# Optimization experiments

Measured on AMD Instinct MI355X. Metric: run time of the kernel, lower is better.

Reference implementation:

```python
import jax, jax.numpy as jnp
import numpy as np

NH = 8       # num_heads
EDIM = 256   # embedding_dim (also per-head dim in this module)
BS, SQL = 4, 1024


def setup_inputs() -> dict:
    key = jax.random.key(0)
    ks = jax.random.split(key, 5)
    scale_in = 1.0 / np.sqrt(EDIM)
    scale_out = 1.0 / np.sqrt(NH * EDIM)
    return {
        "x": jax.random.normal(ks[0], (BS, SQL, EDIM), dtype=jnp.float32),
        "w_attn": jax.random.normal(ks[1], (NH * 3 * EDIM, EDIM), dtype=jnp.float32) * scale_in,
        "b_attn": jax.random.normal(ks[2], (NH * 3 * EDIM,), dtype=jnp.float32) * scale_in,
        "w_out": jax.random.normal(ks[3], (EDIM, NH * EDIM), dtype=jnp.float32) * scale_out,
        "b_out": jax.random.normal(ks[4], (EDIM,), dtype=jnp.float32) * scale_out,
    }


def reference(x, w_attn, b_attn, w_out, b_out):
    bs, sql, edim = x.shape
    nh = NH
    # projections: (bs, sql, nh*3*edim); split into Q, K, V chunks of nh*edim
    proj = x @ w_attn.T + b_attn
    q, k, v = jnp.split(proj, 3, axis=-1)
    # Faithful to torch: raw view (bs, sql, nh*edim) -> (bs, nh, sql, edim),
    # a reinterpretation of memory, NOT a transpose.
    q = q.reshape(bs, nh, sql, edim)
    k = k.reshape(bs, nh, sql, edim)
    v = v.reshape(bs, nh, sql, edim)
    # scaled dot-product scores: (bs, nh, sql, sql)
    scores = jnp.einsum("bhqd,bhkd->bhqk", q, k) / jnp.sqrt(jnp.float32(edim))
    # causal mask: -inf strictly above the diagonal (equivalent to adding triu(-inf, 1))
    causal = jnp.tril(jnp.ones((sql, sql), dtype=bool))
    scores = jnp.where(causal, scores, -jnp.inf)
    attn = jax.nn.softmax(scores, axis=-1)
    out = jnp.einsum("bhqk,bhkd->bhqd", attn, v)
    # Faithful raw view back: (bs, nh, sql, edim) -> (bs, sql, nh*edim)
    out = out.reshape(bs, sql, nh * edim)
    return out @ w_out.T + b_out
```

## Files before the change

### kernel.cpp

```cpp
#include <hip/hip_runtime.h>

#define SQL  1024
#define EDIM 256
#define NHD  8
#define NKV  (NHD * 3 * EDIM)
#define MROWS (4 * SQL)

typedef short bf16x8 __attribute__((ext_vector_type(8)));
typedef float f32x4 __attribute__((ext_vector_type(4)));

__device__ __forceinline__ unsigned short f2bf(float f) {
  unsigned u = __float_as_uint(f);
  u += 0x7fff + ((u >> 16) & 1);
  return (unsigned short)(u >> 16);
}
__device__ __forceinline__ float bf2f(unsigned short s) {
  return __uint_as_float(((unsigned)s) << 16);
}

__device__ __forceinline__ void g2lds16(const void* g, void* l) {
  __builtin_amdgcn_global_load_lds(
      (const __attribute__((address_space(1))) unsigned int*)g,
      (__attribute__((address_space(3))) unsigned int*)l, 16, 0, 0);
}

__device__ __forceinline__ void storev(float* p, float v) { *p = v; }
__device__ __forceinline__ void storev(unsigned short* p, float v) { *p = f2bf(v); }

__global__ __launch_bounds__(256) void cast3_bf16(
    const float* __restrict__ x, unsigned short* __restrict__ xb,
    const float* __restrict__ wa, unsigned short* __restrict__ wb,
    const float* __restrict__ wo, unsigned short* __restrict__ wob) {
  const float* src; unsigned short* dst; int i;
  int blk = blockIdx.x;
  if (blk < 512)       { src = x;  dst = xb;  i = blk * 256 + threadIdx.x; }
  else if (blk < 1280) { src = wa; dst = wb;  i = (blk - 512) * 256 + threadIdx.x; }
  else                 { src = wo; dst = wob; i = (blk - 1280) * 256 + threadIdx.x; }
  float4 a = ((const float4*)src)[2 * i];
  float4 b = ((const float4*)src)[2 * i + 1];
  union { unsigned short s[8]; ulonglong2 v; } u;
  u.s[0] = f2bf(a.x); u.s[1] = f2bf(a.y); u.s[2] = f2bf(a.z); u.s[3] = f2bf(a.w);
  u.s[4] = f2bf(b.x); u.s[5] = f2bf(b.y); u.s[6] = f2bf(b.z); u.s[7] = f2bf(b.w);
  ((ulonglong2*)dst)[i] = u.v;
}

template <int BM, int BN, typename OutT>
__global__ __launch_bounds__(256) void gemm_mfma(
    const unsigned short* __restrict__ A, const unsigned short* __restrict__ B,
    const float* __restrict__ bias, OutT* __restrict__ C,
    int M, int N, int K) {
  constexpr int TM = BM / 32, TN = BN / 32;
  __shared__ __align__(16) unsigned short As[2][BM * 32];
  __shared__ __align__(16) unsigned short Bs[2][BN * 32];
  const int tid = threadIdx.x;
  const int wave = tid >> 6, lane = tid & 63;
  const int quad = lane >> 4, l16 = lane & 15;
  const int wm = (wave >> 1) * (BM / 2), wn = (wave & 1) * (BN / 2);
  const int m0 = blockIdx.x * BM, n0 = blockIdx.y * BN;
  const int sw = (l16 >> 1) & 3;

  f32x4 acc[TM][TN];
  #pragma unroll
  for (int i = 0; i < TM; i++)
    #pragma unroll
    for (int j = 0; j < TN; j++) acc[i][j] = {0.f, 0.f, 0.f, 0.f};

  auto stage = [&](int k0, int bb) {
    #pragma unroll
    for (int it = 0; it < BM / 64; it++) {
      int flat = it * 256 + tid;
      int row = flat >> 2;
      int cg = (flat & 3) ^ ((row >> 1) & 3);
      g2lds16(A + (size_t)(m0 + row) * K + k0 + cg * 8, &As[bb][flat * 8]);
    }
    #pragma unroll
    for (int it = 0; it < BN / 64; it++) {
      int flat = it * 256 + tid;
      int row = flat >> 2;
      int cg = (flat & 3) ^ ((row >> 1) & 3);
      g2lds16(B + (size_t)(n0 + row) * K + k0 + cg * 8, &Bs[bb][flat * 8]);
    }
  };

  stage(0, 0);
  __syncthreads();
  for (int k0 = 0; k0 < K; k0 += 32) {
    const int bb = (k0 >> 5) & 1;
    if (k0 + 32 < K) stage(k0 + 32, bb ^ 1);
    bf16x8 af[TM], bf[TN];
    #pragma unroll
    for (int i = 0; i < TM; i++)
      af[i] = *(const bf16x8*)&As[bb][(wm + i * 16 + l16) * 32 + (quad ^ sw) * 8];
    #pragma unroll
    for (int j = 0; j < TN; j++)
      bf[j] = *(const bf16x8*)&Bs[bb][(wn + j * 16 + l16) * 32 + (quad ^ sw) * 8];
    #pragma unroll
    for (int i = 0; i < TM; i++)
      #pragma unroll
      for (int j = 0; j < TN; j++)
        acc[i][j] = __builtin_amdgcn_mfma_f32_16x16x32_bf16(af[i], bf[j], acc[i][j], 0, 0, 0);
    __syncthreads();
  }

  #pragma unroll
  for (int i = 0; i < TM; i++) {
    #pragma unroll
    for (int r = 0; r < 4; r++) {
      int m = m0 + wm + i * 16 + quad * 4 + r;
      #pragma unroll
      for (int j = 0; j < TN; j++) {
        int n = n0 + wn + j * 16 + l16;
        storev(&C[(size_t)m * N + n], acc[i][j][r] + bias[n]);
      }
    }
  }
}

__global__ __launch_bounds__(256) void transpose_v(
    const unsigned short* __restrict__ proj, unsigned short* __restrict__ vt) {
  __shared__ unsigned short T[64][66];
  const int tid = threadIdx.x;
  const int s0 = blockIdx.x * 64, d0 = blockIdx.y * 64, bh = blockIdx.z;
  const int b = bh >> 3, h = bh & 7;
  #pragma unroll
  for (int it = 0; it < 2; it++) {
    int c = it * 256 + tid;
    int sr = c >> 3, k8 = (c & 7) * 8;
    int s = s0 + sr;
    const unsigned short* src = proj + (size_t)(b * SQL + h * 128 + (s >> 3)) * NKV
                                + 2 * 2048 + (s & 7) * 256 + d0 + k8;
    *(ulonglong2*)&T[sr][k8] = *(const ulonglong2*)src;
  }
  __syncthreads();
  #pragma unroll
  for (int it = 0; it < 2; it++) {
    int c = it * 256 + tid;
    int dr = c >> 3, s8 = (c & 7) * 8;
    unsigned short tmp[8];
    #pragma unroll
    for (int j = 0; j < 8; j++) tmp[j] = T[s8 + j][dr];
    unsigned short* dst = vt + ((size_t)bh * EDIM + d0 + dr) * SQL + s0 + s8;
    *(ulonglong2*)dst = *(ulonglong2*)tmp;
  }
}

__global__ __launch_bounds__(256) void attn_mfma(
    const unsigned short* __restrict__ proj,
    const unsigned short* __restrict__ vt,
    unsigned short* __restrict__ opart,
    float* __restrict__ lpart) {
  __shared__ __align__(16) unsigned short lds[37888];

  const int tid = threadIdx.x;
  const int wave = tid >> 6, lane = tid & 63;
  const int quad = lane >> 4, l16 = lane & 15;
  const int g = blockIdx.x;
  const int bh = g & 31;
  const int t = g >> 5;
  const int qt = (t < 8) ? (7 - t) : (t - 8);
  const int ks = (t < 8) ? 0 : 1;
  const int b = bh >> 3, h = bh & 7;
  const int q0 = qt * 128;
  const int nh = 2 * (qt + 1);
  const int kt0 = ks * nh;
  unsigned short* Ps = lds + 32768 + wave * 1280;

  bf16x8 aq[2][8];
  #pragma unroll
  for (int st = 0; st < 2; st++) {
    int s = q0 + wave * 32 + st * 16 + l16;
    const unsigned short* qrow =
        proj + (size_t)(b * SQL + h * 128 + (s >> 3)) * NKV + (s & 7) * 256;
    #pragma unroll
    for (int kk = 0; kk < 8; kk++)
      aq[st][kk] = *(const bf16x8*)(qrow + kk * 32 + quad * 8);
  }

  auto stage = [&](int kt, int bb) {
    unsigned short* KsB = lds + bb * 8192;
    unsigned short* VtB = lds + 16384 + bb * 8192;
    #pragma unroll
    for (int it = 0; it < 4; it++) {
      int flat = it * 256 + tid;
      int row = flat >> 5, ch = (flat & 31) ^ (row & 7);
      int s = kt * 32 + row;
      g2lds16(proj + (size_t)(b * SQL + h * 128 + (s >> 3)) * NKV + 2048
                   + (s & 7) * 256 + ch * 8,
              KsB + flat * 8);
    }
    #pragma unroll
    for (int it = 0; it < 4; it++) {
      int flat = it * 256 + tid;
      int d = flat >> 2, ch = (flat & 3) ^ ((d >> 1) & 3);
      g2lds16(vt + ((size_t)bh * EDIM + d) * SQL + kt * 32 + ch * 8,
              VtB + flat * 8);
    }
  };

  f32x4 o[2][16];
  #pragma unroll
  for (int st = 0; st < 2; st++)
    #pragma unroll
    for (int tt = 0; tt < 16; tt++) o[st][tt] = {0.f, 0.f, 0.f, 0.f};
  float l_r[2][4] = {};

  stage(kt0, 0);
  __syncthreads();

  for (int i = 0; i < nh; i++) {
    const int kt = kt0 + i;
    const int bb = i & 1;
    if (i + 1 < nh) stage(kt + 1, bb ^ 1);
    const unsigned short* KsB = lds + bb * 8192;
    const unsigned short* VtB = lds + 16384 + bb * 8192;

    f32x4 s[2][2];
    #pragma unroll
    for (int st = 0; st < 2; st++)
      #pragma unroll
      for (int c = 0; c < 2; c++) s[st][c] = {0.f, 0.f, 0.f, 0.f};
    #pragma unroll
    for (int c = 0; c < 2; c++) {
      #pragma unroll
      for (int kk = 0; kk < 8; kk++) {
        int ch = (kk * 4 + quad) ^ (l16 & 7);
        bf16x8 bk = *(const bf16x8*)&KsB[(c * 16 + l16) * 256 + ch * 8];
        s[0][c] = __builtin_amdgcn_mfma_f32_16x16x32_bf16(aq[0][kk], bk, s[0][c], 0, 0, 0);
        s[1][c] = __builtin_amdgcn_mfma_f32_16x16x32_bf16(aq[1][kk], bk, s[1][c], 0, 0, 0);
      }
    }

    #pragma unroll
    for (int st = 0; st < 2; st++) {
      #pragma unroll
      for (int c = 0; c < 2; c++) {
        int kg = kt * 32 + c * 16 + l16;
        #pragma unroll
        for (int r = 0; r < 4; r++) {
          int qg = q0 + wave * 32 + st * 16 + quad * 4 + r;
          float p = (kg <= qg) ? __expf(s[st][c][r] * 0.0625f) : 0.f;
          l_r[st][r] += p;
          Ps[(st * 16 + quad * 4 + r) * 40 + c * 16 + l16] = f2bf(p);
        }
      }
    }

    bf16x8 ap0 = *(const bf16x8*)&Ps[l16 * 40 + quad * 8];
    bf16x8 ap1 = *(const bf16x8*)&Ps[(16 + l16) * 40 + quad * 8];
    #pragma unroll
    for (int tt = 0; tt < 16; tt++) {
      int ch = quad ^ ((l16 >> 1) & 3);
      bf16x8 bv = *(const bf16x8*)&VtB[(tt * 16 + l16) * 32 + ch * 8];
      o[0][tt] = __builtin_amdgcn_mfma_f32_16x16x32_bf16(ap0, bv, o[0][tt], 0, 0, 0);
      o[1][tt] = __builtin_amdgcn_mfma_f32_16x16x32_bf16(ap1, bv, o[1][tt], 0, 0, 0);
    }
    __syncthreads();
  }

  #pragma unroll
  for (int st = 0; st < 2; st++) {
    #pragma unroll
    for (int r = 0; r < 4; r++) {
      float l = l_r[st][r];
      #pragma unroll
      for (int off = 1; off < 16; off <<= 1) l += __shfl_xor(l, off);
      float inv = (l > 0.f) ? 1.0f / l : 0.f;
      int s = q0 + wave * 32 + st * 16 + quad * 4 + r;
      size_t rowidx = (size_t)ks * 32768 + bh * 1024 + s;
      if (l16 == 0) lpart[rowidx] = l;
      unsigned short* dst = opart + rowidx * 256;
      #pragma unroll
      for (int tt = 0; tt < 16; tt++)
        dst[tt * 16 + l16] = f2bf(o[st][tt][r] * inv);
    }
  }
}

__global__ __launch_bounds__(256) void combine_split(
    const unsigned short* __restrict__ opart, const float* __restrict__ lpart,
    unsigned short* __restrict__ obf) {
  int idx = blockIdx.x * 256 + threadIdx.x;
  int row = idx >> 5;
  int oct = idx & 31;
  int bh = row >> 10, s = row & 1023;
  float l1 = lpart[row], l2 = lpart[32768 + row];
  float w = 1.0f / (l1 + l2);
  union { unsigned short s[8]; ulonglong2 v; } u1, u2, uo;
  u1.v = *(const ulonglong2*)(opart + (size_t)row * 256 + oct * 8);
  u2.v = *(const ulonglong2*)(opart + (size_t)(32768 + row) * 256 + oct * 8);
  #pragma unroll
  for (int j = 0; j < 8; j++)
    uo.s[j] = f2bf((bf2f(u1.s[j]) * l1 + bf2f(u2.s[j]) * l2) * w);
  int b = bh >> 3, h = bh & 7;
  unsigned short* dst = obf + (size_t)(b * SQL + h * 128 + (s >> 3)) * 2048
                        + (s & 7) * 256 + oct * 8;
  *(ulonglong2*)dst = uo.v;
}

extern "C" void kernel_launch(void* const* d_in, const int* in_sizes, int n_in,
                              void* d_out, int out_size, void* d_ws, size_t ws_size,
                              hipStream_t stream) {
  const float* x      = (const float*)d_in[0];
  const float* w_attn = (const float*)d_in[1];
  const float* b_attn = (const float*)d_in[2];
  const float* w_out  = (const float*)d_in[3];
  const float* b_out  = (const float*)d_in[4];
  float* out = (float*)d_out;

  char* p = (char*)d_ws;
  unsigned short* proj  = (unsigned short*)p;  p += (size_t)MROWS * NKV * 2;
  unsigned short* obf   = (unsigned short*)p;  p += (size_t)MROWS * 2048 * 2;
  unsigned short* vtb   = (unsigned short*)p;  p += (size_t)32 * EDIM * SQL * 2;
  unsigned short* xb    = (unsigned short*)p;  p += (size_t)MROWS * EDIM * 2;
  unsigned short* wb    = (unsigned short*)p;  p += (size_t)NKV * EDIM * 2;
  unsigned short* wob   = (unsigned short*)p;  p += (size_t)EDIM * 2048 * 2;
  unsigned short* opart = (unsigned short*)p;  p += (size_t)2 * 32768 * 256 * 2;
  float*          lpart = (float*)p;

  cast3_bf16<<<1536, 256, 0, stream>>>(x, xb, w_attn, wb, w_out, wob);
  gemm_mfma<128, 128, unsigned short><<<dim3(MROWS / 128, NKV / 128), 256, 0, stream>>>(
      xb, wb, b_attn, proj, MROWS, NKV, EDIM);
  transpose_v<<<dim3(SQL / 64, EDIM / 64, 32), 256, 0, stream>>>(proj, vtb);
  attn_mfma<<<512, 256, 0, stream>>>(proj, vtb, opart, lpart);
  combine_split<<<4096, 256, 0, stream>>>(opart, lpart, obf);
  gemm_mfma<64, 64, float><<<dim3(MROWS / 64, EDIM / 64), 256, 0, stream>>>(
      obf, wob, b_out, out, MROWS, EDIM, NHD * EDIM);
}
```

Baseline: 195.2 us.

## Balance causal attention work by pairing query tiles and splitting keys evenly

Each causal query tile is paired with its mirror tile (j and 7-j), so every pair covers 36 key tiles in total. That combined key range is split into four equal chunks of 9 tiles, and each block processes one chunk, possibly spanning two query tiles. Partial outputs and row sums go to per-slot buffers, and the combine kernel merges a variable number of partials (up to 4) instead of exactly 2. The goal is to remove the load imbalance where blocks ran between 2 and 16 key tiles. In exchange it adds partial-output traffic, a possible second Q reload per block, and reuses the V-transpose buffer for the combined output.

```diff
diff --git a/kernel.cpp b/kernel.cpp
--- a/kernel.cpp
+++ b/kernel.cpp
@@ -154,26 +154,30 @@
   const int tid = threadIdx.x;
   const int wave = tid >> 6, lane = tid & 63;
   const int quad = lane >> 4, l16 = lane & 15;
+  unsigned short* Ps = lds + 32768 + wave * 1280;
+
   const int g = blockIdx.x;
   const int bh = g & 31;
-  const int t = g >> 5;
-  const int qt = (t < 8) ? (7 - t) : (t - 8);
-  const int ks = (t < 8) ? 0 : 1;
+  const int rem = g >> 5;
+  const int j = rem & 3;
+  const int sb = rem >> 2;
   const int b = bh >> 3, h = bh & 7;
-  const int q0 = qt * 128;
-  const int nh = 2 * (qt + 1);
-  const int kt0 = ks * nh;
-  unsigned short* Ps = lds + 32768 + wave * 1280;
-
-  bf16x8 aq[2][8];
-  #pragma unroll
-  for (int st = 0; st < 2; st++) {
-    int s = q0 + wave * 32 + st * 16 + l16;
-    const unsigned short* qrow =
-        proj + (size_t)(b * SQL + h * 128 + (s >> 3)) * NKV + (s & 7) * 256;
-    #pragma unroll
-    for (int kk = 0; kk < 8; kk++)
-      aq[st][kk] = *(const bf16x8*)(qrow + kk * 32 + quad * 8);
+  const int t0 = 4 * (8 - j);
+  const int m0cnt = (j < 2) ? 4 : 3;
+  const int s1st  = (j < 2) ? 3 : 2;
+  const int lo = 9 * sb, hi = lo + 9;
+
+  int segqt[2], segk0[2], seglen[2], segr[2];
+  int nseg = 0;
+  if (lo < t0) {
+    int e = (hi < t0) ? hi : t0;
+    segqt[nseg] = 7 - j; segk0[nseg] = lo; seglen[nseg] = e - lo;
+    segr[nseg] = sb; nseg++;
+  }
+  if (hi > t0) {
+    int a = (lo > t0) ? lo : t0;
+    segqt[nseg] = j; segk0[nseg] = a - t0; seglen[nseg] = hi - a;
+    segr[nseg] = m0cnt + (sb - s1st); nseg++;
   }
 
   auto stage = [&](int kt, int bb) {
@@ -197,81 +201,98 @@
     }
   };
 
-  f32x4 o[2][16];
-  #pragma unroll
-  for (int st = 0; st < 2; st++)
-    #pragma unroll
-    for (int tt = 0; tt < 16; tt++) o[st][tt] = {0.f, 0.f, 0.f, 0.f};
-  float l_r[2][4] = {};
-
-  stage(kt0, 0);
-  __syncthreads();
-
-  for (int i = 0; i < nh; i++) {
-    const int kt = kt0 + i;
-    const int bb = i & 1;
-    if (i + 1 < nh) stage(kt + 1, bb ^ 1);
-    const unsigned short* KsB = lds + bb * 8192;
-    const unsigned short* VtB = lds + 16384 + bb * 8192;
-
-    f32x4 s[2][2];
+  for (int sg = 0; sg < nseg; sg++) {
+    const int qt = segqt[sg];
+    const int q0 = qt * 128;
+    const int c0 = segk0[sg], len = seglen[sg];
+
+    bf16x8 aq[2][8];
+    #pragma unroll
+    for (int st = 0; st < 2; st++) {
+      int s = q0 + wave * 32 + st * 16 + l16;
+      const unsigned short* qrow =
+          proj + (size_t)(b * SQL + h * 128 + (s >> 3)) * NKV + (s & 7) * 256;
+      #pragma unroll
+      for (int kk = 0; kk < 8; kk++)
+        aq[st][kk] = *(const bf16x8*)(qrow + kk * 32 + quad * 8);
+    }
+
+    f32x4 o[2][16];
     #pragma unroll
     for (int st = 0; st < 2; st++)
       #pragma unroll
-      for (int c = 0; c < 2; c++) s[st][c] = {0.f, 0.f, 0.f, 0.f};
-    #pragma unroll
-    for (int c = 0; c < 2; c++) {
-      #pragma unroll
-      for (int kk = 0; kk < 8; kk++) {
-        int ch = (kk * 4 + quad) ^ (l16 & 7);
-        bf16x8 bk = *(const bf16x8*)&KsB[(c * 16 + l16) * 256 + ch * 8];
-        s[0][c] = __builtin_amdgcn_mfma_f32_16x16x32_bf16(aq[0][kk], bk, s[0][c], 0, 0, 0);
-        s[1][c] = __builtin_amdgcn_mfma_f32_16x16x32_bf16(aq[1][kk], bk, s[1][c], 0, 0, 0);
-      }
-    }
-
+      for (int tt = 0; tt < 16; tt++) o[st][tt] = {0.f, 0.f, 0.f, 0.f};
+    float l_r[2][4] = {};
+
+    stage(c0, 0);
+    __syncthreads();
+
+    for (int i = 0; i < len; i++) {
+      const int kt = c0 + i;
+      const int bb = i & 1;
+      if (i + 1 < len) stage(kt + 1, bb ^ 1);
+      const unsigned short* KsB = lds + bb * 8192;
+      const unsigned short* VtB = lds + 16384 + bb * 8192;
+
+      f32x4 s[2][2];
+      #pragma unroll
+      for (int st = 0; st < 2; st++)
+        #pragma unroll
+        for (int c = 0; c < 2; c++) s[st][c] = {0.f, 0.f, 0.f, 0.f};
+      #pragma unroll
+      for (int c = 0; c < 2; c++) {
+        #pragma unroll
+        for (int kk = 0; kk < 8; kk++) {
+          int ch = (kk * 4 + quad) ^ (l16 & 7);
+          bf16x8 bk = *(const bf16x8*)&KsB[(c * 16 + l16) * 256 + ch * 8];
+          s[0][c] = __builtin_amdgcn_mfma_f32_16x16x32_bf16(aq[0][kk], bk, s[0][c], 0, 0, 0);
+          s[1][c] = __builtin_amdgcn_mfma_f32_16x16x32_bf16(aq[1][kk], bk, s[1][c], 0, 0, 0);
+        }
+      }
+
+      #pragma unroll
+      for (int st = 0; st < 2; st++) {
+        #pragma unroll
+        for (int c = 0; c < 2; c++) {
+          int kg = kt * 32 + c * 16 + l16;
+          #pragma unroll
+          for (int r = 0; r < 4; r++) {
+            int qg = q0 + wave * 32 + st * 16 + quad * 4 + r;
+            float p = (kg <= qg) ? __expf(s[st][c][r] * 0.0625f) : 0.f;
+            l_r[st][r] += p;
+            Ps[(st * 16 + quad * 4 + r) * 40 + c * 16 + l16] = f2bf(p);
+          }
+        }
+      }
+
+      bf16x8 ap0 = *(const bf16x8*)&Ps[l16 * 40 + quad * 8];
+      bf16x8 ap1 = *(const bf16x8*)&Ps[(16 + l16) * 40 + quad * 8];
+      #pragma unroll
+      for (int tt = 0; tt < 16; tt++) {
+        int ch = quad ^ ((l16 >> 1) & 3);
+        bf16x8 bv = *(const bf16x8*)&VtB[(tt * 16 + l16) * 32 + ch * 8];
+        o[0][tt] = __builtin_amdgcn_mfma_f32_16x16x32_bf16(ap0, bv, o[0][tt], 0, 0, 0);
+        o[1][tt] = __builtin_amdgcn_mfma_f32_16x16x32_bf16(ap1, bv, o[1][tt], 0, 0, 0);
+      }
+      __syncthreads();
+    }
+
+    const int slot = (bh * 4 + j) * 5 + segr[sg];
     #pragma unroll
     for (int st = 0; st < 2; st++) {
       #pragma unroll
-      for (int c = 0; c < 2; c++) {
-        int kg = kt * 32 + c * 16 + l16;
-        #pragma unroll
-        for (int r = 0; r < 4; r++) {
-          int qg = q0 + wave * 32 + st * 16 + quad * 4 + r;
-          float p = (kg <= qg) ? __expf(s[st][c][r] * 0.0625f) : 0.f;
-          l_r[st][r] += p;
-          Ps[(st * 16 + quad * 4 + r) * 40 + c * 16 + l16] = f2bf(p);
-        }
-      }
-    }
-
-    bf16x8 ap0 = *(const bf16x8*)&Ps[l16 * 40 + quad * 8];
-    bf16x8 ap1 = *(const bf16x8*)&Ps[(16 + l16) * 40 + quad * 8];
-    #pragma unroll
-    for (int tt = 0; tt < 16; tt++) {
-      int ch = quad ^ ((l16 >> 1) & 3);
-      bf16x8 bv = *(const bf16x8*)&VtB[(tt * 16 + l16) * 32 + ch * 8];
-      o[0][tt] = __builtin_amdgcn_mfma_f32_16x16x32_bf16(ap0, bv, o[0][tt], 0, 0, 0);
-      o[1][tt] = __builtin_amdgcn_mfma_f32_16x16x32_bf16(ap1, bv, o[1][tt], 0, 0, 0);
-    }
-    __syncthreads();
-  }
-
-  #pragma unroll
-  for (int st = 0; st < 2; st++) {
-    #pragma unroll
-    for (int r = 0; r < 4; r++) {
-      float l = l_r[st][r];
-      #pragma unroll
-      for (int off = 1; off < 16; off <<= 1) l += __shfl_xor(l, off);
-      float inv = (l > 0.f) ? 1.0f / l : 0.f;
-      int s = q0 + wave * 32 + st * 16 + quad * 4 + r;
-      size_t rowidx = (size_t)ks * 32768 + bh * 1024 + s;
-      if (l16 == 0) lpart[rowidx] = l;
-      unsigned short* dst = opart + rowidx * 256;
-      #pragma unroll
-      for (int tt = 0; tt < 16; tt++)
-        dst[tt * 16 + l16] = f2bf(o[st][tt][r] * inv);
+      for (int r = 0; r < 4; r++) {
+        float l = l_r[st][r];
+        #pragma unroll
+        for (int off = 1; off < 16; off <<= 1) l += __shfl_xor(l, off);
+        float inv = (l > 0.f) ? 1.0f / l : 0.f;
+        int sl = wave * 32 + st * 16 + quad * 4 + r;
+        if (l16 == 0) lpart[slot * 128 + sl] = l;
+        unsigned short* dst = opart + (size_t)slot * 32768 + sl * 256;
+        #pragma unroll
+        for (int tt = 0; tt < 16; tt++)
+          dst[tt * 16 + l16] = f2bf(o[st][tt][r] * inv);
+      }
     }
   }
 }
@@ -280,17 +301,31 @@
     const unsigned short* __restrict__ opart, const float* __restrict__ lpart,
     unsigned short* __restrict__ obf) {
   int idx = blockIdx.x * 256 + threadIdx.x;
-  int row = idx >> 5;
-  int oct = idx & 31;
+  int row = idx >> 5, oct = idx & 31;
   int bh = row >> 10, s = row & 1023;
-  float l1 = lpart[row], l2 = lpart[32768 + row];
-  float w = 1.0f / (l1 + l2);
-  union { unsigned short s[8]; ulonglong2 v; } u1, u2, uo;
-  u1.v = *(const ulonglong2*)(opart + (size_t)row * 256 + oct * 8);
-  u2.v = *(const ulonglong2*)(opart + (size_t)(32768 + row) * 256 + oct * 8);
-  #pragma unroll
-  for (int j = 0; j < 8; j++)
-    uo.s[j] = f2bf((bf2f(u1.s[j]) * l1 + bf2f(u2.s[j]) * l2) * w);
+  int qt = s >> 7, sl = s & 127;
+  int j, r0, rn;
+  if (qt >= 4) {
+    j = 7 - qt; r0 = 0; rn = (j < 2) ? 4 : 3;
+  } else {
+    j = qt; int m0 = (j < 2) ? 4 : 3; r0 = m0; rn = 5 - m0;
+  }
+  int base = (bh * 4 + j) * 5;
+  float acc[8] = {};
+  float L = 0.f;
+  for (int r = r0; r < r0 + rn; r++) {
+    int slot = base + r;
+    float l = lpart[slot * 128 + sl];
+    L += l;
+    union { unsigned short s[8]; ulonglong2 v; } u;
+    u.v = *(const ulonglong2*)(opart + (size_t)slot * 32768 + sl * 256 + oct * 8);
+    #pragma unroll
+    for (int k = 0; k < 8; k++) acc[k] += bf2f(u.s[k]) * l;
+  }
+  float w = 1.0f / L;
+  union { unsigned short s[8]; ulonglong2 v; } uo;
+  #pragma unroll
+  for (int k = 0; k < 8; k++) uo.s[k] = f2bf(acc[k] * w);
   int b = bh >> 3, h = bh & 7;
   unsigned short* dst = obf + (size_t)(b * SQL + h * 128 + (s >> 3)) * 2048
                         + (s & 7) * 256 + oct * 8;
@@ -309,13 +344,13 @@
 
   char* p = (char*)d_ws;
   unsigned short* proj  = (unsigned short*)p;  p += (size_t)MROWS * NKV * 2;
-  unsigned short* obf   = (unsigned short*)p;  p += (size_t)MROWS * 2048 * 2;
   unsigned short* vtb   = (unsigned short*)p;  p += (size_t)32 * EDIM * SQL * 2;
   unsigned short* xb    = (unsigned short*)p;  p += (size_t)MROWS * EDIM * 2;
   unsigned short* wb    = (unsigned short*)p;  p += (size_t)NKV * EDIM * 2;
   unsigned short* wob   = (unsigned short*)p;  p += (size_t)EDIM * 2048 * 2;
-  unsigned short* opart = (unsigned short*)p;  p += (size_t)2 * 32768 * 256 * 2;
+  unsigned short* opart = (unsigned short*)p;  p += (size_t)640 * 32768 * 2;
   float*          lpart = (float*)p;
+  unsigned short* obf   = vtb;
 
   cast3_bf16<<<1536, 256, 0, stream>>>(x, xb, w_attn, wb, w_out, wob);
   gemm_mfma<128, 128, unsigned short><<<dim3(MROWS / 128, NKV / 128), 256, 0, stream>>>(
```

Measured after the change: 189.1 us. 1.03x faster.
